# Kernel optimization log

Measured on AMD Instinct MI355X. Metric: run time of the kernel, lower is better.

## Reference

```python
import math
import jax, jax.numpy as jnp
import numpy as np

C, H, W, G = 256, 56, 56, 8
CG = C // G  # channels per group


def setup_inputs() -> dict:
    key = jax.random.key(0)
    ks = jax.random.split(key, 8)
    n = 32
    x = jax.random.normal(ks[0], (n, C, H, W), dtype=jnp.float32)
    # p_3: 1x1 conv (out=C, in=C)
    Wp3 = jax.random.normal(ks[1], (C, C), dtype=jnp.float32) * (1.0 / math.sqrt(C))
    bp3 = jnp.zeros((C,), dtype=jnp.float32)
    # pj_1 / pj_2: grouped 1x1 convs, groups=8 -> (G, out_per_group, in_per_group)
    Wg1 = jax.random.normal(ks[2], (G, CG, CG), dtype=jnp.float32) * (1.0 / math.sqrt(CG))
    bg1 = jnp.zeros((C,), dtype=jnp.float32)
    Wg2 = jax.random.normal(ks[3], (G, CG, CG), dtype=jnp.float32) * (1.0 / math.sqrt(CG))
    bg2 = jnp.zeros((C,), dtype=jnp.float32)
    # p_7_w: trunc_normal(std=0.02), plain normal is fine for a reference
    p7w = jax.random.normal(ks[4], (1, C, C), dtype=jnp.float32) * 0.02
    return {"x": x, "Wp3": Wp3, "bp3": bp3, "Wg1": Wg1, "bg1": bg1,
            "Wg2": Wg2, "bg2": bg2, "p7w": p7w}


def _conv1x1(x, Wm, b):
    # x: [n,C,H,W], Wm: [C_out, C_in]
    return jnp.einsum('oi,nihw->nohw', Wm, x) + b[None, :, None, None]


def _grouped_conv1x1(x, Wg, b):
    # x: [n,C,H,W] -> [n,G,CG,H,W]; Wg: [G, out_pg, in_pg]
    n = x.shape[0]
    xg = x.reshape(n, G, CG, H, W)
    yg = jnp.einsum('goi,ngihw->ngohw', Wg, xg)
    return yg.reshape(n, C, H, W) + b[None, :, None, None]


def reference(x, Wp3, bp3, Wg1, bg1, Wg2, bg2, p7w):
    n = x.shape[0]
    hw = H * W
    t3 = _conv1x1(x, Wp3, bp3)                        # [n,C,H,W]
    t4 = jnp.sin(x * (math.pi / 2))                   # [n,C,H,W]
    lhs = _grouped_conv1x1(x, Wg1, bg1).reshape(n, C, hw)
    rhs = _grouped_conv1x1(x, Wg2, bg2).reshape(n, C, hw)
    # channel-channel attention: [n,C,C]
    t5 = jnp.einsum('ncx,ndx->ncd', lhs, rhs) / math.sqrt(hw)
    t6 = jnp.maximum(t3, t4).reshape(n, C, hw)        # [n,C,HW]
    t7 = p7w * t5                                     # [n,C,C]
    # bmm: [n,HW,C] @ [n,C,C] -> [n,HW,C]
    t8 = jnp.einsum('ncx,ncd->nxd', t6, t7) / math.sqrt(C)
    # [n,H,W,C] -> [n,C,H,W]
    return t8.reshape(n, H, W, C).transpose(0, 3, 1, 2)
```

## Files before the change

### kernel.cpp

```cpp
#include <hip/hip_runtime.h>
#include <hip/hip_bf16.h>

#define NB 32
#define CD 256
#define HW 3136
#define XP 3200
#define NQ 4

typedef __bf16 bf16;
typedef __attribute__((ext_vector_type(8))) __bf16 bf16x8;
typedef __attribute__((ext_vector_type(4))) float f32x4;

__device__ __forceinline__ void gload_lds16(const void* g, void* l) {
  __builtin_amdgcn_global_load_lds((const __attribute__((address_space(1))) void*)g,
                                   (__attribute__((address_space(3))) void*)l,
                                   16, 0, 0);
}

__global__ __launch_bounds__(256) void k_prep(const float* __restrict__ x,
                                              bf16* __restrict__ xT,
                                              bf16* __restrict__ sT,
                                              bf16* __restrict__ xbf,
                                              float* __restrict__ rsum) {
  const int b = blockIdx.z, pxt = blockIdx.x, cht = blockIdx.y;
  const int t = threadIdx.x;
  const int px0 = pxt * 64, c0 = cht * 64;
  bf16* xTb = xT + (size_t)b * XP * CD;
  bf16* sTb = sT + (size_t)b * XP * CD;
  if (pxt == 49) {
    const int j = t >> 2, q = t & 3;
    uint4 z = {};
    uint4* d1 = (uint4*)(xTb + (size_t)(px0 + j) * CD + c0 + q * 16);
    uint4* d2 = (uint4*)(sTb + (size_t)(px0 + j) * CD + c0 + q * 16);
    d1[0] = z; d1[1] = z; d2[0] = z; d2[1] = z;
    return;
  }
  __shared__ float tile[64][65];
  const float* xb = x + (size_t)b * CD * HW;
  bf16* xbfb = xbf + (size_t)b * CD * HW;
  const int i0 = t >> 4, j4 = (t & 15) * 4;
#pragma unroll
  for (int it = 0; it < 4; ++it) {
    int i = it * 16 + i0;
    float4 v = *(const float4*)(xb + (size_t)(c0 + i) * HW + px0 + j4);
    tile[i][j4] = v.x; tile[i][j4 + 1] = v.y; tile[i][j4 + 2] = v.z; tile[i][j4 + 3] = v.w;
    bf16 o4[4] = {(bf16)v.x, (bf16)v.y, (bf16)v.z, (bf16)v.w};
    *(uint2*)(xbfb + (size_t)(c0 + i) * HW + px0 + j4) = *(uint2*)o4;
  }
  __syncthreads();
  {
    const int i = t >> 2, js = (t & 3) * 16;
    float p = 0.f;
#pragma unroll
    for (int k = 0; k < 16; ++k) p += tile[i][js + k];
    p += __shfl_xor(p, 1);
    p += __shfl_xor(p, 2);
    if ((t & 3) == 0) atomicAdd(rsum + b * CD + c0 + i, p);
  }
  const int j = t >> 2, q = t & 3;
  bf16 xo[16], so[16];
#pragma unroll
  for (int k = 0; k < 16; ++k) {
    float v = tile[q * 16 + k][j];
    xo[k] = (bf16)v;
    so[k] = (bf16)__sinf(v * 1.57079632679489662f);
  }
  bf16x8* d1 = (bf16x8*)(xTb + (size_t)(px0 + j) * CD + c0 + q * 16);
  bf16x8* d2 = (bf16x8*)(sTb + (size_t)(px0 + j) * CD + c0 + q * 16);
  d1[0] = ((bf16x8*)xo)[0]; d1[1] = ((bf16x8*)xo)[1];
  d2[0] = ((bf16x8*)so)[0]; d2[1] = ((bf16x8*)so)[1];
}

__global__ __launch_bounds__(256) void k_wcvt(const float* __restrict__ w,
                                              bf16* __restrict__ wb) {
  int i = (blockIdx.x * 256 + threadIdx.x) * 4;
  float4 v = *(const float4*)(w + i);
  bf16 o[4] = {(bf16)v.x, (bf16)v.y, (bf16)v.z, (bf16)v.w};
  *(uint2*)(wb + i) = *(uint2*)o;
}

__global__ __launch_bounds__(512) void k_gram(const bf16* __restrict__ xbf,
                                              float* __restrict__ Gpart) {
  __shared__ __attribute__((aligned(16))) char sm[32 * 1024];
  bf16* smA = (bf16*)sm;
  bf16* smB = (bf16*)(sm + 16384);
  const int bz = blockIdx.z, b = bz >> 2, q = bz & 3;
  const int mt = blockIdx.x, nt = blockIdx.y;
  const int t = threadIdx.x, w = t >> 6, l = t & 63;
  const int wr = w >> 2, wc = w & 3, lrow = l & 15, lk = l >> 4;
  const bf16* Ab = xbf + (size_t)b * CD * HW + (size_t)(mt * 128) * HW;
  const bf16* Bb = xbf + (size_t)b * CD * HW + (size_t)(nt * 128) * HW;
  const int it0 = q * 13, it1 = (q == 3) ? 49 : (q * 13 + 13);
  const f32x4 z4 = {0.f, 0.f, 0.f, 0.f};
  f32x4 acc[4][2];
#pragma unroll
  for (int m = 0; m < 4; ++m) { acc[m][0] = z4; acc[m][1] = z4; }
  for (int it = it0; it < it1; ++it) {
    const int kt = it * 64;
#pragma unroll
    for (int rr = 0; rr < 2; ++rr) {
      int chunk = rr * 512 + t;
      int row = chunk >> 3, cb = (chunk & 7) * 16;
      int kb = cb ^ ((row & 7) << 4);
      gload_lds16(Ab + (size_t)row * HW + kt + (kb >> 1), sm + chunk * 16);
    }
#pragma unroll
    for (int rr = 0; rr < 2; ++rr) {
      int chunk = rr * 512 + t;
      int row = chunk >> 3, cb = (chunk & 7) * 16;
      int kb = cb ^ ((row & 7) << 4);
      gload_lds16(Bb + (size_t)row * HW + kt + (kb >> 1), sm + 16384 + chunk * 16);
    }
    __syncthreads();
#pragma unroll
    for (int kk = 0; kk < 64; kk += 32) {
      bf16x8 af[4], bfv[2];
#pragma unroll
      for (int m = 0; m < 4; ++m) {
        int row = wr * 64 + m * 16 + lrow;
        int cb = (kk * 2 + lk * 16) ^ ((row & 7) << 4);
        af[m] = *(const bf16x8*)(sm + row * 128 + cb);
      }
#pragma unroll
      for (int n = 0; n < 2; ++n) {
        int row = wc * 32 + n * 16 + lrow;
        int cb = (kk * 2 + lk * 16) ^ ((row & 7) << 4);
        bfv[n] = *(const bf16x8*)(sm + 16384 + row * 128 + cb);
      }
#pragma unroll
      for (int m = 0; m < 4; ++m)
#pragma unroll
        for (int n = 0; n < 2; ++n)
          acc[m][n] = __builtin_amdgcn_mfma_f32_16x16x32_bf16(af[m], bfv[n], acc[m][n], 0, 0, 0);
    }
    __syncthreads();
  }
  float* Gp = Gpart + ((size_t)q * NB + b) * CD * CD + (size_t)(mt * 128) * CD + nt * 128;
#pragma unroll
  for (int m = 0; m < 4; ++m)
#pragma unroll
    for (int n = 0; n < 2; ++n) {
      int col = wc * 32 + n * 16 + lrow;
#pragma unroll
      for (int r = 0; r < 4; ++r) {
        int c = wr * 64 + m * 16 + lk * 4 + r;
        Gp[(size_t)c * CD + col] = acc[m][n][r];
      }
    }
}

__global__ __launch_bounds__(256) void k_t7(const float* __restrict__ Gpart,
                                            const float* __restrict__ Wg1,
                                            const float* __restrict__ bg1,
                                            const float* __restrict__ Wg2,
                                            const float* __restrict__ bg2,
                                            const float* __restrict__ rsum,
                                            const float* __restrict__ p7w,
                                            bf16* __restrict__ t7T) {
  const int gd = blockIdx.x, b = blockIdx.y, t = threadIdx.x;
  __shared__ float Tm[32][256];
  __shared__ float W2t[32][32];
  __shared__ float rb[256];
  __shared__ float u2s[32];
  float gv[32], w1v[32];
#pragma unroll
  for (int j = 0; j < 32; ++j) gv[j] = 0.f;
  for (int q = 0; q < NQ; ++q) {
    const float* Gp = Gpart + ((size_t)q * NB + b) * CD * CD + (size_t)t * CD + gd * 32;
#pragma unroll
    for (int j = 0; j < 32; ++j) gv[j] += Gp[j];
  }
  {
    const float* w1p = Wg1 + t * 32;
#pragma unroll
    for (int i = 0; i < 32; ++i) w1v[i] = w1p[i];
  }
  rb[t] = rsum[b * CD + t];
  if (t < 32) {
    const float* w2p = Wg2 + gd * 1024 + t * 32;
#pragma unroll
    for (int j = 0; j < 32; ++j) W2t[j][t] = w2p[j];
  }
  __syncthreads();
  if (t < 32) {
    float u = 0.f;
#pragma unroll
    for (int j = 0; j < 32; ++j) u += W2t[j][t] * rb[gd * 32 + j];
    u2s[t] = u;
  }
#pragma unroll
  for (int dp = 0; dp < 32; ++dp) {
    float s = 0.f;
#pragma unroll
    for (int j = 0; j < 32; ++j) s += gv[j] * W2t[j][dp];
    Tm[dp][t] = s;
  }
  __syncthreads();
  const int gc = t >> 5;
  float u1c = 0.f;
#pragma unroll
  for (int i = 0; i < 32; ++i) u1c += w1v[i] * rb[gc * 32 + i];
  const float b1c = bg1[t];
  bf16* outb = t7T + (size_t)b * CD * CD;
  const float* p7p = p7w + (size_t)t * CD + gd * 32;
#pragma unroll
  for (int dp = 0; dp < 32; ++dp) {
    float mv = 0.f;
#pragma unroll
    for (int i = 0; i < 32; ++i) mv += w1v[i] * Tm[dp][gc * 32 + i];
    int d = gd * 32 + dp;
    float b2d = bg2[d];
    float tv = mv + u1c * b2d + b1c * u2s[dp] + 3136.f * b1c * b2d;
    float t7v = tv * (p7p[dp] * (1.f / 896.f));
    outb[(size_t)d * CD + t] = (bf16)t7v;
  }
}

__global__ __launch_bounds__(512) void k_gemm1(const bf16* __restrict__ xT,
                                               const bf16* __restrict__ Wp3b,
                                               const float* __restrict__ bp3,
                                               const bf16* __restrict__ sT,
                                               bf16* __restrict__ t6T) {
  __shared__ __attribute__((aligned(16))) char sm[48 * 1024];
  const int b = blockIdx.z, mt = blockIdx.x;
  const int t = threadIdx.x, w = t >> 6, l = t & 63;
  const int wr = w >> 2, wc = w & 3, lrow = l & 15, lk = l >> 4;
  const bf16* Ab = xT + (size_t)b * XP * CD + (size_t)(mt * 128) * CD;
  const bf16* Bb = Wp3b;
  const f32x4 z4 = {0.f, 0.f, 0.f, 0.f};
  f32x4 acc[4][4];
#pragma unroll
  for (int m = 0; m < 4; ++m)
#pragma unroll
    for (int n = 0; n < 4; ++n) acc[m][n] = z4;
  for (int kt = 0; kt < CD; kt += 64) {
#pragma unroll
    for (int rr = 0; rr < 2; ++rr) {
      int chunk = rr * 512 + t;
      int row = chunk >> 3, cb = (chunk & 7) * 16;
      int kb = cb ^ ((row & 7) << 4);
      gload_lds16(Ab + (size_t)row * CD + kt + (kb >> 1), sm + chunk * 16);
    }
#pragma unroll
    for (int rr = 0; rr < 4; ++rr) {
      int chunk = rr * 512 + t;
      int row = chunk >> 3, cb = (chunk & 7) * 16;
      int kb = cb ^ ((row & 7) << 4);
      gload_lds16(Bb + (size_t)row * CD + kt + (kb >> 1), sm + 16384 + chunk * 16);
    }
    __syncthreads();
#pragma unroll
    for (int kk = 0; kk < 64; kk += 32) {
      bf16x8 af[4], bfv[4];
#pragma unroll
      for (int m = 0; m < 4; ++m) {
        int row = wr * 64 + m * 16 + lrow;
        int cb = (kk * 2 + lk * 16) ^ ((row & 7) << 4);
        af[m] = *(const bf16x8*)(sm + row * 128 + cb);
      }
#pragma unroll
      for (int n = 0; n < 4; ++n) {
        int row = wc * 64 + n * 16 + lrow;
        int cb = (kk * 2 + lk * 16) ^ ((row & 7) << 4);
        bfv[n] = *(const bf16x8*)(sm + 16384 + row * 128 + cb);
      }
#pragma unroll
      for (int m = 0; m < 4; ++m)
#pragma unroll
        for (int n = 0; n < 4; ++n)
          acc[m][n] = __builtin_amdgcn_mfma_f32_16x16x32_bf16(af[m], bfv[n], acc[m][n], 0, 0, 0);
    }
    __syncthreads();
  }
  bf16* outb = t6T + (size_t)b * XP * CD;
  const bf16* sTb = sT + (size_t)b * XP * CD;
#pragma unroll
  for (int h = 0; h < 2; ++h) {
    __syncthreads();
    if ((wc >> 1) == h) {
#pragma unroll
      for (int m = 0; m < 4; ++m)
#pragma unroll
        for (int n = 0; n < 4; ++n) {
          int o = wc * 64 + n * 16 + lrow;
          int col = o - h * 128;
          float bias = bp3[o];
#pragma unroll
          for (int r = 0; r < 4; ++r) {
            int row = wr * 64 + m * 16 + lk * 4 + r;
            int ba = row * 256 + ((col * 2) ^ (((row >> 2) & 3) << 4));
            *(bf16*)(sm + ba) = (bf16)(acc[m][n][r] + bias);
          }
        }
    }
    __syncthreads();
#pragma unroll
    for (int it = 0; it < 4; ++it) {
      int chunk = it * 512 + t;
      int row = chunk >> 4;
      int cb16 = (chunk & 15) * 16;
      int ba = row * 256 + (cb16 ^ (((row >> 2) & 3) << 4));
      bf16x8 v = *(const bf16x8*)(sm + ba);
      size_t gi = (size_t)(mt * 128 + row) * CD + h * 128 + (chunk & 15) * 8;
      bf16x8 sv = *(const bf16x8*)(sTb + gi);
      bf16x8 ov;
#pragma unroll
      for (int e = 0; e < 8; ++e) {
        float a = (float)v[e], s = (float)sv[e];
        ov[e] = (bf16)fmaxf(a, s);
      }
      *(bf16x8*)(outb + gi) = ov;
    }
  }
}

__global__ __launch_bounds__(512) void k_gemm3(const bf16* __restrict__ t7T,
                                               const bf16* __restrict__ t6T,
                                               float* __restrict__ out) {
  __shared__ __attribute__((aligned(16))) char sm[48 * 1024];
  const int b = blockIdx.z, xt = blockIdx.x;
  const int t = threadIdx.x, w = t >> 6, l = t & 63;
  const int wr = w >> 1, wc = w & 1, lrow = l & 15, lk = l >> 4;
  const bf16* Ab = t7T + (size_t)b * CD * CD;
  const bf16* Bb = t6T + (size_t)b * XP * CD + (size_t)(xt * 128) * CD;
  const f32x4 z4 = {0.f, 0.f, 0.f, 0.f};
  f32x4 acc[4][4];
#pragma unroll
  for (int m = 0; m < 4; ++m)
#pragma unroll
    for (int n = 0; n < 4; ++n) acc[m][n] = z4;
  for (int kt = 0; kt < CD; kt += 64) {
#pragma unroll
    for (int rr = 0; rr < 4; ++rr) {
      int chunk = rr * 512 + t;
      int row = chunk >> 3, cb = (chunk & 7) * 16;
      int kb = cb ^ ((row & 7) << 4);
      gload_lds16(Ab + (size_t)row * CD + kt + (kb >> 1), sm + chunk * 16);
    }
#pragma unroll
    for (int rr = 0; rr < 2; ++rr) {
      int chunk = rr * 512 + t;
      int row = chunk >> 3, cb = (chunk & 7) * 16;
      int kb = cb ^ ((row & 7) << 4);
      gload_lds16(Bb + (size_t)row * CD + kt + (kb >> 1), sm + 32768 + chunk * 16);
    }
    __syncthreads();
#pragma unroll
    for (int kk = 0; kk < 64; kk += 32) {
      bf16x8 af[4], bfv[4];
#pragma unroll
      for (int m = 0; m < 4; ++m) {
        int row = wr * 64 + m * 16 + lrow;
        int cb = (kk * 2 + lk * 16) ^ ((row & 7) << 4);
        af[m] = *(const bf16x8*)(sm + row * 128 + cb);
      }
#pragma unroll
      for (int n = 0; n < 4; ++n) {
        int row = wc * 64 + n * 16 + lrow;
        int cb = (kk * 2 + lk * 16) ^ ((row & 7) << 4);
        bfv[n] = *(const bf16x8*)(sm + 32768 + row * 128 + cb);
      }
#pragma unroll
      for (int m = 0; m < 4; ++m)
#pragma unroll
        for (int n = 0; n < 4; ++n)
          acc[m][n] = __builtin_amdgcn_mfma_f32_16x16x32_bf16(af[m], bfv[n], acc[m][n], 0, 0, 0);
    }
    __syncthreads();
  }
  float* ob = out + (size_t)b * CD * HW;
#pragma unroll
  for (int m = 0; m < 4; ++m)
#pragma unroll
    for (int n = 0; n < 4; ++n) {
      int xcol = xt * 128 + wc * 64 + n * 16 + lrow;
      if (xcol < HW) {
#pragma unroll
        for (int r = 0; r < 4; ++r) {
          int d = wr * 64 + m * 16 + lk * 4 + r;
          ob[(size_t)d * HW + xcol] = acc[m][n][r];
        }
      }
    }
}

extern "C" void kernel_launch(void* const* d_in, const int* in_sizes, int n_in,
                              void* d_out, int out_size, void* d_ws, size_t ws_size,
                              hipStream_t stream) {
  const float* x   = (const float*)d_in[0];
  const float* Wp3 = (const float*)d_in[1];
  const float* bp3 = (const float*)d_in[2];
  const float* Wg1 = (const float*)d_in[3];
  const float* bg1 = (const float*)d_in[4];
  const float* Wg2 = (const float*)d_in[5];
  const float* bg2 = (const float*)d_in[6];
  const float* p7w = (const float*)d_in[7];
  float* out = (float*)d_out;

  char* ws = (char*)d_ws;
  bf16*  xT    = (bf16*)(ws);
  bf16*  sT    = (bf16*)(ws + 52428800);
  bf16*  xbf   = (bf16*)(ws + 104857600);
  float* Gpart = (float*)(ws + 156237824);
  bf16*  t7T   = (bf16*)(ws + 189792256);
  bf16*  Wp3b  = (bf16*)(ws + 193986560);
  float* rsum  = (float*)(ws + 194117632);
  bf16*  t6T   = (bf16*)(ws + 104857600);

  hipMemsetAsync(rsum, 0, NB * CD * sizeof(float), stream);
  k_wcvt<<<dim3(64), 256, 0, stream>>>(Wp3, Wp3b);
  k_prep<<<dim3(50, 4, NB), 256, 0, stream>>>(x, xT, sT, xbf, rsum);
  k_gram<<<dim3(2, 2, NB * NQ), 512, 0, stream>>>(xbf, Gpart);
  k_t7<<<dim3(8, NB), 256, 0, stream>>>(Gpart, Wg1, bg1, Wg2, bg2, rsum, p7w, t7T);
  k_gemm1<<<dim3(25, 1, NB), 512, 0, stream>>>(xT, Wp3b, bp3, sT, t6T);
  k_gemm3<<<dim3(25, 1, NB), 512, 0, stream>>>(t7T, t6T, out);
}
```

Before: 335.5 us.

## Drop sin and bf16 intermediates; compute sin in GEMM epilogue, Gram from fp32

Stops materialising two workspace tensors: the bf16 sin tensor and the channel-major bf16 copy of x. Sin is now computed in the first GEMM's epilogue from the transposed bf16 x, and the Gram kernel reads fp32 x directly, converts it to bf16 into LDS, and register-prefetches the next K slice. Each Gram block now computes a 128x256 strip using all channels held in LDS. This removes large intermediate writes and reads, in exchange for more fp32 reads in the Gram kernel and extra sin work in the GEMM epilogue.

```diff
diff --git a/kernel.cpp b/kernel.cpp
--- a/kernel.cpp
+++ b/kernel.cpp
@@ -19,33 +19,26 @@
 
 __global__ __launch_bounds__(256) void k_prep(const float* __restrict__ x,
                                               bf16* __restrict__ xT,
-                                              bf16* __restrict__ sT,
-                                              bf16* __restrict__ xbf,
                                               float* __restrict__ rsum) {
   const int b = blockIdx.z, pxt = blockIdx.x, cht = blockIdx.y;
   const int t = threadIdx.x;
   const int px0 = pxt * 64, c0 = cht * 64;
   bf16* xTb = xT + (size_t)b * XP * CD;
-  bf16* sTb = sT + (size_t)b * XP * CD;
   if (pxt == 49) {
     const int j = t >> 2, q = t & 3;
     uint4 z = {};
     uint4* d1 = (uint4*)(xTb + (size_t)(px0 + j) * CD + c0 + q * 16);
-    uint4* d2 = (uint4*)(sTb + (size_t)(px0 + j) * CD + c0 + q * 16);
-    d1[0] = z; d1[1] = z; d2[0] = z; d2[1] = z;
+    d1[0] = z; d1[1] = z;
     return;
   }
   __shared__ float tile[64][65];
   const float* xb = x + (size_t)b * CD * HW;
-  bf16* xbfb = xbf + (size_t)b * CD * HW;
   const int i0 = t >> 4, j4 = (t & 15) * 4;
 #pragma unroll
   for (int it = 0; it < 4; ++it) {
     int i = it * 16 + i0;
     float4 v = *(const float4*)(xb + (size_t)(c0 + i) * HW + px0 + j4);
     tile[i][j4] = v.x; tile[i][j4 + 1] = v.y; tile[i][j4 + 2] = v.z; tile[i][j4 + 3] = v.w;
-    bf16 o4[4] = {(bf16)v.x, (bf16)v.y, (bf16)v.z, (bf16)v.w};
-    *(uint2*)(xbfb + (size_t)(c0 + i) * HW + px0 + j4) = *(uint2*)o4;
   }
   __syncthreads();
   {
@@ -58,17 +51,11 @@
     if ((t & 3) == 0) atomicAdd(rsum + b * CD + c0 + i, p);
   }
   const int j = t >> 2, q = t & 3;
-  bf16 xo[16], so[16];
-#pragma unroll
-  for (int k = 0; k < 16; ++k) {
-    float v = tile[q * 16 + k][j];
-    xo[k] = (bf16)v;
-    so[k] = (bf16)__sinf(v * 1.57079632679489662f);
-  }
+  bf16 xo[16];
+#pragma unroll
+  for (int k = 0; k < 16; ++k) xo[k] = (bf16)tile[q * 16 + k][j];
   bf16x8* d1 = (bf16x8*)(xTb + (size_t)(px0 + j) * CD + c0 + q * 16);
-  bf16x8* d2 = (bf16x8*)(sTb + (size_t)(px0 + j) * CD + c0 + q * 16);
   d1[0] = ((bf16x8*)xo)[0]; d1[1] = ((bf16x8*)xo)[1];
-  d2[0] = ((bf16x8*)so)[0]; d2[1] = ((bf16x8*)so)[1];
 }
 
 __global__ __launch_bounds__(256) void k_wcvt(const float* __restrict__ w,
@@ -79,72 +66,78 @@
   *(uint2*)(wb + i) = *(uint2*)o;
 }
 
-__global__ __launch_bounds__(512) void k_gram(const bf16* __restrict__ xbf,
+#define GRAM_LOAD(ITV)                                                  \
+  {                                                                     \
+    const int kt = (ITV) * 64;                                          \
+    _Pragma("unroll")                                                   \
+    for (int s8 = 0; s8 < 8; ++s8) {                                    \
+      int s = s8 * 512 + t;                                             \
+      int c = s >> 4, p4 = s & 15;                                      \
+      rv[s8] = *(const float4*)(xb + (size_t)c * HW + kt + p4 * 4);     \
+    }                                                                   \
+  }
+
+__global__ __launch_bounds__(512) void k_gram(const float* __restrict__ x,
                                               float* __restrict__ Gpart) {
   __shared__ __attribute__((aligned(16))) char sm[32 * 1024];
-  bf16* smA = (bf16*)sm;
-  bf16* smB = (bf16*)(sm + 16384);
-  const int bz = blockIdx.z, b = bz >> 2, q = bz & 3;
-  const int mt = blockIdx.x, nt = blockIdx.y;
+  const int b = blockIdx.z, q = blockIdx.y, mt = blockIdx.x;
   const int t = threadIdx.x, w = t >> 6, l = t & 63;
   const int wr = w >> 2, wc = w & 3, lrow = l & 15, lk = l >> 4;
-  const bf16* Ab = xbf + (size_t)b * CD * HW + (size_t)(mt * 128) * HW;
-  const bf16* Bb = xbf + (size_t)b * CD * HW + (size_t)(nt * 128) * HW;
-  const int it0 = q * 13, it1 = (q == 3) ? 49 : (q * 13 + 13);
+  const float* xb = x + (size_t)b * CD * HW;
+  const int it0 = (q * 49) / NQ, it1 = ((q + 1) * 49) / NQ;
   const f32x4 z4 = {0.f, 0.f, 0.f, 0.f};
-  f32x4 acc[4][2];
-#pragma unroll
-  for (int m = 0; m < 4; ++m) { acc[m][0] = z4; acc[m][1] = z4; }
+  f32x4 acc[4][4];
+#pragma unroll
+  for (int m = 0; m < 4; ++m)
+#pragma unroll
+    for (int n = 0; n < 4; ++n) acc[m][n] = z4;
+
+  float4 rv[8];
+  GRAM_LOAD(it0);
   for (int it = it0; it < it1; ++it) {
-    const int kt = it * 64;
-#pragma unroll
-    for (int rr = 0; rr < 2; ++rr) {
-      int chunk = rr * 512 + t;
-      int row = chunk >> 3, cb = (chunk & 7) * 16;
-      int kb = cb ^ ((row & 7) << 4);
-      gload_lds16(Ab + (size_t)row * HW + kt + (kb >> 1), sm + chunk * 16);
-    }
-#pragma unroll
-    for (int rr = 0; rr < 2; ++rr) {
-      int chunk = rr * 512 + t;
-      int row = chunk >> 3, cb = (chunk & 7) * 16;
-      int kb = cb ^ ((row & 7) << 4);
-      gload_lds16(Bb + (size_t)row * HW + kt + (kb >> 1), sm + 16384 + chunk * 16);
-    }
-    __syncthreads();
+#pragma unroll
+    for (int s8 = 0; s8 < 8; ++s8) {
+      int s = s8 * 512 + t;
+      int c = s >> 4, p4 = s & 15;
+      bf16 o4[4] = {(bf16)rv[s8].x, (bf16)rv[s8].y, (bf16)rv[s8].z, (bf16)rv[s8].w};
+      int ba = c * 128 + ((p4 * 8) ^ ((c & 7) << 4));
+      *(uint2*)(sm + ba) = *(uint2*)o4;
+    }
+    __syncthreads();
+    if (it + 1 < it1) GRAM_LOAD(it + 1);
 #pragma unroll
     for (int kk = 0; kk < 64; kk += 32) {
-      bf16x8 af[4], bfv[2];
+      bf16x8 af[4], bfv[4];
 #pragma unroll
       for (int m = 0; m < 4; ++m) {
-        int row = wr * 64 + m * 16 + lrow;
-        int cb = (kk * 2 + lk * 16) ^ ((row & 7) << 4);
-        af[m] = *(const bf16x8*)(sm + row * 128 + cb);
-      }
-#pragma unroll
-      for (int n = 0; n < 2; ++n) {
-        int row = wc * 32 + n * 16 + lrow;
-        int cb = (kk * 2 + lk * 16) ^ ((row & 7) << 4);
-        bfv[n] = *(const bf16x8*)(sm + 16384 + row * 128 + cb);
+        int row = mt * 128 + wr * 64 + m * 16 + lrow;
+        int ba = row * 128 + ((kk * 2 + lk * 16) ^ ((row & 7) << 4));
+        af[m] = *(const bf16x8*)(sm + ba);
+      }
+#pragma unroll
+      for (int n = 0; n < 4; ++n) {
+        int row = wc * 64 + n * 16 + lrow;
+        int ba = row * 128 + ((kk * 2 + lk * 16) ^ ((row & 7) << 4));
+        bfv[n] = *(const bf16x8*)(sm + ba);
       }
 #pragma unroll
       for (int m = 0; m < 4; ++m)
 #pragma unroll
-        for (int n = 0; n < 2; ++n)
+        for (int n = 0; n < 4; ++n)
           acc[m][n] = __builtin_amdgcn_mfma_f32_16x16x32_bf16(af[m], bfv[n], acc[m][n], 0, 0, 0);
     }
     __syncthreads();
   }
-  float* Gp = Gpart + ((size_t)q * NB + b) * CD * CD + (size_t)(mt * 128) * CD + nt * 128;
+  float* Gp = Gpart + ((size_t)q * NB + b) * CD * CD + (size_t)(mt * 128) * CD;
 #pragma unroll
   for (int m = 0; m < 4; ++m)
 #pragma unroll
-    for (int n = 0; n < 2; ++n) {
-      int col = wc * 32 + n * 16 + lrow;
+    for (int n = 0; n < 4; ++n) {
+      int d = wc * 64 + n * 16 + lrow;
 #pragma unroll
       for (int r = 0; r < 4; ++r) {
         int c = wr * 64 + m * 16 + lk * 4 + r;
-        Gp[(size_t)c * CD + col] = acc[m][n][r];
+        Gp[(size_t)c * CD + d] = acc[m][n][r];
       }
     }
 }
@@ -219,13 +212,13 @@
 __global__ __launch_bounds__(512) void k_gemm1(const bf16* __restrict__ xT,
                                                const bf16* __restrict__ Wp3b,
                                                const float* __restrict__ bp3,
-                                               const bf16* __restrict__ sT,
                                                bf16* __restrict__ t6T) {
   __shared__ __attribute__((aligned(16))) char sm[48 * 1024];
   const int b = blockIdx.z, mt = blockIdx.x;
   const int t = threadIdx.x, w = t >> 6, l = t & 63;
   const int wr = w >> 2, wc = w & 3, lrow = l & 15, lk = l >> 4;
-  const bf16* Ab = xT + (size_t)b * XP * CD + (size_t)(mt * 128) * CD;
+  const bf16* xTb = xT + (size_t)b * XP * CD;
+  const bf16* Ab = xTb + (size_t)(mt * 128) * CD;
   const bf16* Bb = Wp3b;
   const f32x4 z4 = {0.f, 0.f, 0.f, 0.f};
   f32x4 acc[4][4];
@@ -273,7 +266,6 @@
     __syncthreads();
   }
   bf16* outb = t6T + (size_t)b * XP * CD;
-  const bf16* sTb = sT + (size_t)b * XP * CD;
 #pragma unroll
   for (int h = 0; h < 2; ++h) {
     __syncthreads();
@@ -302,11 +294,12 @@
       int ba = row * 256 + (cb16 ^ (((row >> 2) & 3) << 4));
       bf16x8 v = *(const bf16x8*)(sm + ba);
       size_t gi = (size_t)(mt * 128 + row) * CD + h * 128 + (chunk & 15) * 8;
-      bf16x8 sv = *(const bf16x8*)(sTb + gi);
+      bf16x8 xv = *(const bf16x8*)(xTb + gi);
       bf16x8 ov;
 #pragma unroll
       for (int e = 0; e < 8; ++e) {
-        float a = (float)v[e], s = (float)sv[e];
+        float a = (float)v[e];
+        float s = __sinf((float)xv[e] * 1.57079632679489662f);
         ov[e] = (bf16)fmaxf(a, s);
       }
       *(bf16x8*)(outb + gi) = ov;
@@ -399,19 +392,17 @@
 
   char* ws = (char*)d_ws;
   bf16*  xT    = (bf16*)(ws);
-  bf16*  sT    = (bf16*)(ws + 52428800);
-  bf16*  xbf   = (bf16*)(ws + 104857600);
-  float* Gpart = (float*)(ws + 156237824);
-  bf16*  t7T   = (bf16*)(ws + 189792256);
-  bf16*  Wp3b  = (bf16*)(ws + 193986560);
-  float* rsum  = (float*)(ws + 194117632);
-  bf16*  t6T   = (bf16*)(ws + 104857600);
+  bf16*  t6T   = (bf16*)(ws + 52428800);
+  float* Gpart = (float*)(ws + 104857600);
+  bf16*  t7T   = (bf16*)(ws + 138412032);
+  bf16*  Wp3b  = (bf16*)(ws + 142606336);
+  float* rsum  = (float*)(ws + 142737408);
 
   hipMemsetAsync(rsum, 0, NB * CD * sizeof(float), stream);
   k_wcvt<<<dim3(64), 256, 0, stream>>>(Wp3, Wp3b);
-  k_prep<<<dim3(50, 4, NB), 256, 0, stream>>>(x, xT, sT, xbf, rsum);
-  k_gram<<<dim3(2, 2, NB * NQ), 512, 0, stream>>>(xbf, Gpart);
+  k_prep<<<dim3(50, 4, NB), 256, 0, stream>>>(x, xT, rsum);
+  k_gram<<<dim3(2, NQ, NB), 512, 0, stream>>>(x, Gpart);
   k_t7<<<dim3(8, NB), 256, 0, stream>>>(Gpart, Wg1, bg1, Wg2, bg2, rsum, p7w, t7T);
-  k_gemm1<<<dim3(25, 1, NB), 512, 0, stream>>>(xT, Wp3b, bp3, sT, t6T);
+  k_gemm1<<<dim3(25, 1, NB), 512, 0, stream>>>(xT, Wp3b, bp3, t6T);
   k_gemm3<<<dim3(25, 1, NB), 512, 0, stream>>>(t7T, t6T, out);
 }
```

Measured after the change: 310.6 us. 7.4% less time.
